# Optimization experiments

Hardware: AMD Instinct MI355X
Metric: run time of the kernel (lower is better)

Reference implementation:

```python
import jax, jax.numpy as jnp
import numpy as np

N_NODES = 100000
N_EDGES = 1600000
IN_F = 64
HID_F = 64
HID_CH = 32
OUT_F = 16


def setup_inputs() -> dict:
    key = jax.random.key(0)
    ks = jax.random.split(key, 12)
    feat = jax.random.normal(ks[0], (N_NODES, IN_F), dtype=jnp.float32)
    edge_src = jax.random.randint(ks[1], (N_EDGES,), 0, N_NODES, dtype=jnp.int32)
    edge_dst = jax.random.randint(ks[2], (N_EDGES,), 0, N_NODES, dtype=jnp.int32)
    s = 1.414 / np.sqrt(IN_F)
    fc1_w = jax.random.normal(ks[3], (HID_F, IN_F), dtype=jnp.float32) * s
    fc1_b = jnp.zeros((HID_F,), dtype=jnp.float32)
    filt_w = jax.random.normal(ks[4], (HID_F, IN_F), dtype=jnp.float32) * s
    filt_b = jnp.zeros((HID_F,), dtype=jnp.float32)
    att_w1 = jax.random.normal(ks[5], (HID_F, HID_CH), dtype=jnp.float32) * (1.0 / np.sqrt(HID_F))
    att_b1 = jnp.zeros((HID_CH,), dtype=jnp.float32)
    att_w2 = jax.random.normal(ks[6], (HID_CH, 1), dtype=jnp.float32) * (1.0 / np.sqrt(HID_CH))
    fc2_w = jax.random.normal(ks[7], (OUT_F, HID_F), dtype=jnp.float32) * (1.414 / np.sqrt(HID_F))
    fc2_b = jnp.zeros((OUT_F,), dtype=jnp.float32)
    return {
        "feat": feat, "edge_src": edge_src, "edge_dst": edge_dst,
        "fc1_w": fc1_w, "fc1_b": fc1_b, "filt_w": filt_w, "filt_b": filt_b,
        "att_w1": att_w1, "att_b1": att_b1, "att_w2": att_w2,
        "fc2_w": fc2_w, "fc2_b": fc2_b,
    }


def _lp_filter(feat, edge_src, edge_dst, filt_w, filt_b):
    # Low-pass (GCN-style) filter: symmetric-normalized neighborhood aggregation
    # of the linearly transformed features.  x: [N, H]
    x = feat @ filt_w.T + filt_b
    ones = jnp.ones((edge_src.shape[0],), dtype=x.dtype)
    deg_out = jax.ops.segment_sum(ones, edge_src, num_segments=N_NODES)
    deg_in = jax.ops.segment_sum(ones, edge_dst, num_segments=N_NODES)
    inv_sqrt_out = jax.lax.rsqrt(jnp.maximum(deg_out, 1.0))
    inv_sqrt_in = jax.lax.rsqrt(jnp.maximum(deg_in, 1.0))
    # gather-transform-scatter: msg_e = x[src_e] * norm_e  ->  sum at dst
    coef = inv_sqrt_out[edge_src] * inv_sqrt_in[edge_dst]  # [E]
    msg = x[edge_src] * coef[:, None]                       # [E, H]
    return jax.ops.segment_sum(msg, edge_dst, num_segments=N_NODES)  # [N, H]


def _channel_attention(z, att_w1, att_b1, att_w2):
    # z: [N, C, H]; semantic (channel) attention a la HAN
    w = jnp.tanh(z @ att_w1 + att_b1) @ att_w2        # [N, C, 1]
    beta = jax.nn.softmax(w.mean(axis=0), axis=0)     # [C, 1]
    return (beta[None, :, :] * z).sum(axis=1)         # [N, H]


def reference(feat, edge_src, edge_dst, fc1_w, fc1_b, filt_w, filt_b,
              att_w1, att_b1, att_w2, fc2_w, fc2_b):
    h1 = jnp.tanh(feat @ fc1_w.T + fc1_b)                          # MLP branch [N, H]
    h2 = _lp_filter(feat, edge_src, edge_dst, filt_w, filt_b)      # graph branch [N, H]
    z = jnp.stack([h1, h2], axis=1)                                # [N, 2, H]
    fused = _channel_attention(z, att_w1, att_b1, att_w2)          # [N, H]
    return fused @ fc2_w.T + fc2_b                                 # [N, OUT_F]
```

## Files before the change

### kernel.cpp

```cpp
#include <hip/hip_runtime.h>
#include <math.h>

#define N_NODESC 100000
#define N_EDGESC 1600000
#define NBUCK 1563
#define BSLACK 1280
#define SCHUNK 4096
#define NSBLK 391

__device__ __forceinline__ float fast_tanh(float x) {
    float ax = fabsf(x);
    float e = __expf(-2.f * ax);
    float r = (1.f - e) * __builtin_amdgcn_rcpf(1.f + e);
    return copysignf(r, x);
}

__global__ void binit_kernel(int* __restrict__ bcur) {
    int i = blockIdx.x * blockDim.x + threadIdx.x;
    if (i < NBUCK) bcur[i] = i * BSLACK;
}

__global__ __launch_bounds__(256) void gemm_kernel(
    const float* __restrict__ feat,
    const float* __restrict__ w1, const float* __restrict__ b1,
    const float* __restrict__ w2, const float* __restrict__ b2,
    const int* __restrict__ deg_out,
    float* __restrict__ h1, float* __restrict__ xs) {
    __shared__ float sf[128 * 68];
    int tid = threadIdx.x;
    int base = blockIdx.x * 128;
    for (int k = 0; k < 8; k++) {
        int fi = tid + k * 256;
        int node = fi >> 4, f4 = fi & 15;
        float4 v = make_float4(0.f, 0.f, 0.f, 0.f);
        if (base + node < N_NODESC)
            v = ((const float4*)feat)[(size_t)(base + node) * 16 + f4];
        float* d = &sf[node * 68 + f4 * 4];
        d[0] = v.x; d[1] = v.y; d[2] = v.z; d[3] = v.w;
    }
    __syncthreads();

    int lane = tid & 63;
    int og = __builtin_amdgcn_readfirstlane(tid >> 6);
    const float* wp1 = w1 + og * 16 * 64;
    const float* wp2 = w2 + og * 16 * 64;

    float a1[2][16], a2[2][16];
#pragma unroll
    for (int o = 0; o < 16; o++) {
        float bb1 = b1[og * 16 + o], bb2 = b2[og * 16 + o];
        a1[0][o] = bb1; a1[1][o] = bb1;
        a2[0][o] = bb2; a2[1][o] = bb2;
    }

    for (int fq = 0; fq < 16; fq++) {
        float4 fv0 = *(const float4*)&sf[lane * 68 + fq * 4];
        float4 fv1 = *(const float4*)&sf[(lane + 64) * 68 + fq * 4];
#pragma unroll
        for (int o = 0; o < 16; o++) {
            float4 wv1 = *(const float4*)&wp1[o * 64 + fq * 4];
            float4 wv2 = *(const float4*)&wp2[o * 64 + fq * 4];
            a1[0][o] += fv0.x * wv1.x + fv0.y * wv1.y + fv0.z * wv1.z + fv0.w * wv1.w;
            a1[1][o] += fv1.x * wv1.x + fv1.y * wv1.y + fv1.z * wv1.z + fv1.w * wv1.w;
            a2[0][o] += fv0.x * wv2.x + fv0.y * wv2.y + fv0.z * wv2.z + fv0.w * wv2.w;
            a2[1][o] += fv1.x * wv2.x + fv1.y * wv2.y + fv1.z * wv2.z + fv1.w * wv2.w;
        }
    }

#pragma unroll
    for (int j = 0; j < 2; j++) {
        int g = base + lane + j * 64;
        if (g >= N_NODESC) continue;
        float is = rsqrtf(fmaxf((float)deg_out[g], 1.f));
#pragma unroll
        for (int oq = 0; oq < 4; oq++) {
            float4 t, u;
            t.x = fast_tanh(a1[j][oq * 4 + 0]); t.y = fast_tanh(a1[j][oq * 4 + 1]);
            t.z = fast_tanh(a1[j][oq * 4 + 2]); t.w = fast_tanh(a1[j][oq * 4 + 3]);
            u.x = a2[j][oq * 4 + 0] * is;   u.y = a2[j][oq * 4 + 1] * is;
            u.z = a2[j][oq * 4 + 2] * is;   u.w = a2[j][oq * 4 + 3] * is;
            ((float4*)h1)[(size_t)g * 16 + og * 4 + oq] = t;
            ((float4*)xs)[(size_t)g * 16 + og * 4 + oq] = u;
        }
    }
}

__global__ __launch_bounds__(1024) void scatter2_kernel(const int* __restrict__ src,
                                                        const int* __restrict__ dst,
                                                        int* __restrict__ bcur,
                                                        unsigned* __restrict__ bedges,
                                                        int* __restrict__ deg_out) {
    __shared__ int hist[NBUCK];
    int tid = threadIdx.x;
    int e_beg = blockIdx.x * SCHUNK;
    int e_end = min(e_beg + SCHUNK, N_EDGESC);
    for (int i = tid; i < NBUCK; i += 1024) hist[i] = 0;
    __syncthreads();
#pragma unroll 4
    for (int i = e_beg + tid; i < e_end; i += 1024)
        atomicAdd(&hist[dst[i] >> 6], 1);
    __syncthreads();
    for (int i = tid; i < NBUCK; i += 1024) {
        int c = hist[i];
        if (c > 0) hist[i] = atomicAdd(&bcur[i], c);
    }
    __syncthreads();
#pragma unroll 4
    for (int i = e_beg + tid; i < e_end; i += 1024) {
        int s = src[i], d = dst[i];
        atomicAdd(&deg_out[s], 1);
        int slot = atomicAdd(&hist[d >> 6], 1);
        bedges[slot] = (unsigned)s | ((unsigned)(d & 63) << 17);
    }
}

__global__ __launch_bounds__(256) void agg4_kernel(const int* __restrict__ bcur,
                                                   const unsigned* __restrict__ bedges,
                                                   const float* __restrict__ xs,
                                                   float* __restrict__ h2) {
    __shared__ unsigned eraw[BSLACK];
    __shared__ unsigned eled[BSLACK];
    __shared__ int loff[65];
    __shared__ int lcnt[64];
    __shared__ int lcur[64];
    int tid = threadIdx.x, lane = tid & 63, wid = tid >> 6;
    int b = blockIdx.x;
    int beg = b * BSLACK;
    int m = bcur[b] - beg;

    if (tid < 64) lcnt[tid] = 0;
    __syncthreads();
    for (int i = tid; i < m; i += 256) {
        unsigned pk = bedges[beg + i];
        eraw[i] = pk;
        atomicAdd(&lcnt[pk >> 17], 1);
    }
    __syncthreads();
    if (wid == 0) {
        int c = lcnt[lane];
        int v = c;
#pragma unroll
        for (int off = 1; off < 64; off <<= 1) {
            int t = __shfl_up(v, off, 64);
            if (lane >= off) v += t;
        }
        loff[lane] = v - c;
        lcur[lane] = v - c;
        if (lane == 63) loff[64] = v;
    }
    __syncthreads();
    for (int i = tid; i < m; i += 256) {
        unsigned pk = eraw[i];
        int pos = atomicAdd(&lcur[pk >> 17], 1);
        eled[pos] = pk & 0x1FFFFu;
    }
    __syncthreads();

    int nbase = b * 64;
#pragma unroll 1
    for (int t = 0; t < 16; t++) {
        int nl = wid * 16 + t;
        int s0 = loff[nl], s1 = loff[nl + 1];
        float acc = 0.f;
        for (int k = s0; k < s1; k += 16) {
            int cnt = s1 - k; if (cnt > 16) cnt = 16;
            unsigned sv = eled[min(k + (lane & 15), s1 - 1)];
            float v[16];
#pragma unroll
            for (int j = 0; j < 16; j++) {
                if (j < cnt) {
                    int sj = __shfl((int)sv, j, 64);
                    v[j] = xs[(size_t)sj * 64 + lane];
                }
            }
#pragma unroll
            for (int j = 0; j < 16; j++)
                if (j < cnt) acc += v[j];
        }
        int g = nbase + nl;
        if (g < N_NODESC) {
            float isq = rsqrtf(fmaxf((float)(s1 - s0), 1.f));
            h2[(size_t)g * 64 + lane] = acc * isq;
        }
    }
}

__global__ __launch_bounds__(256) void att_kernel(const float* __restrict__ h1,
                                                  const float* __restrict__ h2,
                                                  const float* __restrict__ aw1,
                                                  const float* __restrict__ ab1,
                                                  const float* __restrict__ aw2,
                                                  float* __restrict__ wsum) {
    __shared__ float sw1[64 * 32];
    __shared__ float sb1[32];
    __shared__ float sw2[32];
    int tid = threadIdx.x;
    for (int i = tid; i < 64 * 32; i += 256) sw1[i] = aw1[i];
    if (tid < 32) { sb1[tid] = ab1[tid]; sw2[tid] = aw2[tid]; }
    __syncthreads();

    int n = blockIdx.x * 256 + tid;
    float sc[2] = {0.f, 0.f};
    if (n < N_NODESC) {
#pragma unroll
        for (int c = 0; c < 2; c++) {
            const float* row = (c == 0 ? h1 : h2) + (size_t)n * 64;
            float acc[32];
#pragma unroll
            for (int k = 0; k < 32; k++) acc[k] = sb1[k];
            for (int fq = 0; fq < 16; fq++) {
                float4 rv = ((const float4*)row)[fq];
#pragma unroll
                for (int k = 0; k < 32; k++) {
                    acc[k] += rv.x * sw1[(fq * 4 + 0) * 32 + k]
                            + rv.y * sw1[(fq * 4 + 1) * 32 + k]
                            + rv.z * sw1[(fq * 4 + 2) * 32 + k]
                            + rv.w * sw1[(fq * 4 + 3) * 32 + k];
                }
            }
            float s = 0.f;
#pragma unroll
            for (int k = 0; k < 32; k++) s += fast_tanh(acc[k]) * sw2[k];
            sc[c] = s;
        }
    }
#pragma unroll
    for (int off = 32; off; off >>= 1) {
        sc[0] += __shfl_down(sc[0], off, 64);
        sc[1] += __shfl_down(sc[1], off, 64);
    }
    if ((threadIdx.x & 63) == 0) {
        atomicAdd(&wsum[0], sc[0]);
        atomicAdd(&wsum[1], sc[1]);
    }
}

__global__ void beta_kernel(const float* __restrict__ wsum, float* __restrict__ beta) {
    float w0 = wsum[0] / (float)N_NODESC, w1 = wsum[1] / (float)N_NODESC;
    float m = fmaxf(w0, w1);
    float e0 = expf(w0 - m), e1 = expf(w1 - m);
    float inv = 1.f / (e0 + e1);
    beta[0] = e0 * inv;
    beta[1] = e1 * inv;
}

__global__ __launch_bounds__(256) void out_kernel(const float* __restrict__ h1,
                                                  const float* __restrict__ h2,
                                                  const float* __restrict__ beta,
                                                  const float* __restrict__ w,
                                                  const float* __restrict__ b,
                                                  float* __restrict__ out) {
    __shared__ float sw[16 * 68];
    int tid = threadIdx.x;
    {
        int o = tid >> 4, f4 = tid & 15;
        float4 v = ((const float4*)w)[tid];
        float* d = &sw[o * 68 + f4 * 4];
        d[0] = v.x; d[1] = v.y; d[2] = v.z; d[3] = v.w;
    }
    __syncthreads();
    int o = tid & 15, ln = tid >> 4;
    int node = blockIdx.x * 16 + ln;
    if (node >= N_NODESC) return;
    float b0 = beta[0], b1v = beta[1];
    const float4* r1 = (const float4*)(h1 + (size_t)node * 64);
    const float4* r2 = (const float4*)(h2 + (size_t)node * 64);
    float acc = b[o];
    for (int fq = 0; fq < 16; fq++) {
        float4 x1 = r1[fq], x2 = r2[fq];
        float4 wv = *(const float4*)&sw[o * 68 + fq * 4];
        acc += (b0 * x1.x + b1v * x2.x) * wv.x + (b0 * x1.y + b1v * x2.y) * wv.y
             + (b0 * x1.z + b1v * x2.z) * wv.z + (b0 * x1.w + b1v * x2.w) * wv.w;
    }
    out[(size_t)node * 16 + o] = acc;
}

extern "C" void kernel_launch(void* const* d_in, const int* in_sizes, int n_in,
                              void* d_out, int out_size, void* d_ws, size_t ws_size,
                              hipStream_t stream) {
    (void)in_sizes; (void)n_in; (void)out_size; (void)ws_size;
    const float* feat = (const float*)d_in[0];
    const int*   esrc = (const int*)d_in[1];
    const int*   edst = (const int*)d_in[2];
    const float* fc1w = (const float*)d_in[3];
    const float* fc1b = (const float*)d_in[4];
    const float* fltw = (const float*)d_in[5];
    const float* fltb = (const float*)d_in[6];
    const float* aw1  = (const float*)d_in[7];
    const float* ab1  = (const float*)d_in[8];
    const float* aw2  = (const float*)d_in[9];
    const float* fc2w = (const float*)d_in[10];
    const float* fc2b = (const float*)d_in[11];
    float* out = (float*)d_out;

    char* ws = (char*)d_ws;
    size_t off = 0;
    auto alloc = [&](size_t bytes) {
        char* p = ws + off;
        off += (bytes + 255) & ~(size_t)255;
        return p;
    };
    float*    h1      = (float*)alloc((size_t)N_NODESC * 64 * 4);
    float*    xs      = (float*)alloc((size_t)N_NODESC * 64 * 4);
    float*    h2      = (float*)alloc((size_t)N_NODESC * 64 * 4);
    int*      deg_out = (int*)alloc((size_t)N_NODESC * 4);
    int*      bcur    = (int*)alloc((size_t)NBUCK * 4);
    unsigned* bedges  = (unsigned*)alloc((size_t)NBUCK * BSLACK * 4);
    float*    wsum    = (float*)alloc(16 * 4);
    float*    beta    = (float*)alloc(16 * 4);

    hipMemsetAsync(deg_out, 0, (size_t)N_NODESC * 4, stream);
    hipMemsetAsync(wsum, 0, 2 * 4, stream);

    binit_kernel<<<(NBUCK + 255) / 256, 256, 0, stream>>>(bcur);
    scatter2_kernel<<<NSBLK, 1024, 0, stream>>>(esrc, edst, bcur, bedges, deg_out);
    gemm_kernel<<<(N_NODESC + 127) / 128, 256, 0, stream>>>(
        feat, fc1w, fc1b, fltw, fltb, deg_out, h1, xs);
    agg4_kernel<<<NBUCK, 256, 0, stream>>>(bcur, bedges, xs, h2);
    att_kernel<<<(N_NODESC + 255) / 256, 256, 0, stream>>>(h1, h2, aw1, ab1, aw2, wsum);
    beta_kernel<<<1, 1, 0, stream>>>(wsum, beta);
    out_kernel<<<(N_NODESC + 15) / 16, 256, 0, stream>>>(h1, h2, beta, fc2w, fc2b, out);
}
```

Measured before the change: 362.7 us.

## Replace global out-degree atomics with source-bucketed byte lists counted in shared memory

The scatter kernel no longer does a global atomicAdd per edge into deg_out. It now also bins each edge by source bucket, writing a one-byte local source index per edge into a second slack-bucketed array. The GEMM kernel then rebuilds each node's out-degree with shared-memory atomics over its two source buckets, which also removes the deg_out memset. Edge loads are staged in registers so src/dst are read once instead of twice. The cost is a second histogram, more shared-memory atomics, an extra byte-array write and read, and an extra barrier in the GEMM.

```diff
diff --git a/kernel.cpp b/kernel.cpp
--- a/kernel.cpp
+++ b/kernel.cpp
@@ -15,20 +15,67 @@
     return copysignf(r, x);
 }
 
-__global__ void binit_kernel(int* __restrict__ bcur) {
+__global__ void binit_kernel(int* __restrict__ bcur, int* __restrict__ sbcur) {
     int i = blockIdx.x * blockDim.x + threadIdx.x;
-    if (i < NBUCK) bcur[i] = i * BSLACK;
+    if (i < NBUCK) { bcur[i] = i * BSLACK; sbcur[i] = i * BSLACK; }
+}
+
+__global__ __launch_bounds__(1024) void scatter_dual_kernel(
+    const int* __restrict__ src, const int* __restrict__ dst,
+    int* __restrict__ bcur, int* __restrict__ sbcur,
+    unsigned* __restrict__ bedges, unsigned char* __restrict__ sbytes) {
+    __shared__ int histd[NBUCK];
+    __shared__ int hists[NBUCK];
+    int tid = threadIdx.x;
+    int e_beg = blockIdx.x * SCHUNK;
+    int e_end = min(e_beg + SCHUNK, N_EDGESC);
+    for (int i = tid; i < NBUCK; i += 1024) { histd[i] = 0; hists[i] = 0; }
+    __syncthreads();
+
+    int ss[4], dd[4];
+    int cnt = 0;
+    for (int i = e_beg + tid; i < e_end; i += 1024) {
+        ss[cnt] = src[i];
+        dd[cnt] = dst[i];
+        cnt++;
+    }
+#pragma unroll
+    for (int j = 0; j < 4; j++) {
+        if (j < cnt) {
+            atomicAdd(&histd[dd[j] >> 6], 1);
+            atomicAdd(&hists[ss[j] >> 6], 1);
+        }
+    }
+    __syncthreads();
+    for (int i = tid; i < NBUCK; i += 1024) {
+        int c = histd[i];
+        if (c > 0) histd[i] = atomicAdd(&bcur[i], c);
+        int c2 = hists[i];
+        if (c2 > 0) hists[i] = atomicAdd(&sbcur[i], c2);
+    }
+    __syncthreads();
+#pragma unroll
+    for (int j = 0; j < 4; j++) {
+        if (j < cnt) {
+            int slot = atomicAdd(&histd[dd[j] >> 6], 1);
+            bedges[slot] = (unsigned)ss[j] | ((unsigned)(dd[j] & 63) << 17);
+            int slot2 = atomicAdd(&hists[ss[j] >> 6], 1);
+            sbytes[slot2] = (unsigned char)(ss[j] & 63);
+        }
+    }
 }
 
 __global__ __launch_bounds__(256) void gemm_kernel(
     const float* __restrict__ feat,
     const float* __restrict__ w1, const float* __restrict__ b1,
     const float* __restrict__ w2, const float* __restrict__ b2,
-    const int* __restrict__ deg_out,
+    const int* __restrict__ sbcur, const unsigned char* __restrict__ sbytes,
     float* __restrict__ h1, float* __restrict__ xs) {
     __shared__ float sf[128 * 68];
+    __shared__ int ldeg[128];
     int tid = threadIdx.x;
     int base = blockIdx.x * 128;
+    if (tid < 128) ldeg[tid] = 0;
     for (int k = 0; k < 8; k++) {
         int fi = tid + k * 256;
         int node = fi >> 4, f4 = fi & 15;
@@ -40,6 +87,17 @@
     }
     __syncthreads();
 
+#pragma unroll
+    for (int h = 0; h < 2; h++) {
+        int sb = blockIdx.x * 2 + h;
+        if (sb < NBUCK) {
+            int sbeg = sb * BSLACK;
+            int sm = sbcur[sb] - sbeg;
+            for (int i = tid; i < sm; i += 256)
+                atomicAdd(&ldeg[h * 64 + (int)sbytes[sbeg + i]], 1);
+        }
+    }
+
     int lane = tid & 63;
     int og = __builtin_amdgcn_readfirstlane(tid >> 6);
     const float* wp1 = w1 + og * 16 * 64;
@@ -67,11 +125,13 @@
         }
     }
 
+    __syncthreads();
+
 #pragma unroll
     for (int j = 0; j < 2; j++) {
         int g = base + lane + j * 64;
         if (g >= N_NODESC) continue;
-        float is = rsqrtf(fmaxf((float)deg_out[g], 1.f));
+        float is = rsqrtf(fmaxf((float)ldeg[j * 64 + lane], 1.f));
 #pragma unroll
         for (int oq = 0; oq < 4; oq++) {
             float4 t, u;
@@ -82,35 +142,6 @@
             ((float4*)h1)[(size_t)g * 16 + og * 4 + oq] = t;
             ((float4*)xs)[(size_t)g * 16 + og * 4 + oq] = u;
         }
-    }
-}
-
-__global__ __launch_bounds__(1024) void scatter2_kernel(const int* __restrict__ src,
-                                                        const int* __restrict__ dst,
-                                                        int* __restrict__ bcur,
-                                                        unsigned* __restrict__ bedges,
-                                                        int* __restrict__ deg_out) {
-    __shared__ int hist[NBUCK];
-    int tid = threadIdx.x;
-    int e_beg = blockIdx.x * SCHUNK;
-    int e_end = min(e_beg + SCHUNK, N_EDGESC);
-    for (int i = tid; i < NBUCK; i += 1024) hist[i] = 0;
-    __syncthreads();
-#pragma unroll 4
-    for (int i = e_beg + tid; i < e_end; i += 1024)
-        atomicAdd(&hist[dst[i] >> 6], 1);
-    __syncthreads();
-    for (int i = tid; i < NBUCK; i += 1024) {
-        int c = hist[i];
-        if (c > 0) hist[i] = atomicAdd(&bcur[i], c);
-    }
-    __syncthreads();
-#pragma unroll 4
-    for (int i = e_beg + tid; i < e_end; i += 1024) {
-        int s = src[i], d = dst[i];
-        atomicAdd(&deg_out[s], 1);
-        int slot = atomicAdd(&hist[d >> 6], 1);
-        bedges[slot] = (unsigned)s | ((unsigned)(d & 63) << 17);
     }
 }
 
@@ -300,22 +331,23 @@
         off += (bytes + 255) & ~(size_t)255;
         return p;
     };
-    float*    h1      = (float*)alloc((size_t)N_NODESC * 64 * 4);
-    float*    xs      = (float*)alloc((size_t)N_NODESC * 64 * 4);
-    float*    h2      = (float*)alloc((size_t)N_NODESC * 64 * 4);
-    int*      deg_out = (int*)alloc((size_t)N_NODESC * 4);
-    int*      bcur    = (int*)alloc((size_t)NBUCK * 4);
-    unsigned* bedges  = (unsigned*)alloc((size_t)NBUCK * BSLACK * 4);
-    float*    wsum    = (float*)alloc(16 * 4);
-    float*    beta    = (float*)alloc(16 * 4);
-
-    hipMemsetAsync(deg_out, 0, (size_t)N_NODESC * 4, stream);
+    float*         h1     = (float*)alloc((size_t)N_NODESC * 64 * 4);
+    float*         xs     = (float*)alloc((size_t)N_NODESC * 64 * 4);
+    float*         h2     = (float*)alloc((size_t)N_NODESC * 64 * 4);
+    int*           bcur   = (int*)alloc((size_t)NBUCK * 4);
+    int*           sbcur  = (int*)alloc((size_t)NBUCK * 4);
+    unsigned*      bedges = (unsigned*)alloc((size_t)NBUCK * BSLACK * 4);
+    unsigned char* sbytes = (unsigned char*)alloc((size_t)NBUCK * BSLACK);
+    float*         wsum   = (float*)alloc(16 * 4);
+    float*         beta   = (float*)alloc(16 * 4);
+
     hipMemsetAsync(wsum, 0, 2 * 4, stream);
 
-    binit_kernel<<<(NBUCK + 255) / 256, 256, 0, stream>>>(bcur);
-    scatter2_kernel<<<NSBLK, 1024, 0, stream>>>(esrc, edst, bcur, bedges, deg_out);
+    binit_kernel<<<(NBUCK + 255) / 256, 256, 0, stream>>>(bcur, sbcur);
+    scatter_dual_kernel<<<NSBLK, 1024, 0, stream>>>(esrc, edst, bcur, sbcur,
+                                                    bedges, sbytes);
     gemm_kernel<<<(N_NODESC + 127) / 128, 256, 0, stream>>>(
-        feat, fc1w, fc1b, fltw, fltb, deg_out, h1, xs);
+        feat, fc1w, fc1b, fltw, fltb, sbcur, sbytes, h1, xs);
     agg4_kernel<<<NBUCK, 256, 0, stream>>>(bcur, bedges, xs, h2);
     att_kernel<<<(N_NODESC + 255) / 256, 256, 0, stream>>>(h1, h2, aw1, ab1, aw2, wsum);
     beta_kernel<<<1, 1, 0, stream>>>(wsum, beta);
```

New measurement: 322.4 us. 1.13x faster.
